# Kernel optimization log

Measured on AMD Instinct MI355X. Metric: run time of the kernel, lower is better.

The kernel has to match this reference:

```python
import jax, jax.numpy as jnp
import numpy as np
from jax import lax

HEADS = 8
WIN_SIZES = (2, 4, 8)


def _linear(x, w, b):
    return x @ w + b


def _window_attention(x2d, ws, w4, b4):
    # x2d: (B,H,W,C); w4: (4,C,C) = [q,k,v,out]; b4: (4,C)
    B, H, W, C = x2d.shape
    p1, p2 = H // ws, W // ws
    xw = x2d.reshape(B, p1, ws, p2, ws, C).transpose(0, 1, 3, 2, 4, 5)
    xw = xw.reshape(B, p1, p2, ws * ws, C)
    hs = C // HEADS
    q = _linear(xw, w4[0], b4[0]).reshape(B, p1, p2, ws * ws, HEADS, hs)
    k = _linear(xw, w4[1], b4[1]).reshape(B, p1, p2, ws * ws, HEADS, hs)
    v = _linear(xw, w4[2], b4[2]).reshape(B, p1, p2, ws * ws, HEADS, hs)
    scores = jnp.einsum('bpqwhd,bpqvhd->bpqhwv', q, k) / jnp.sqrt(jnp.asarray(hs, x2d.dtype))
    probs = jax.nn.softmax(scores, axis=-1)
    ctx = jnp.einsum('bpqhwv,bpqvhd->bpqwhd', probs, v).reshape(B, p1, p2, ws * ws, C)
    return _linear(ctx, w4[3], b4[3])


def _unwindow(out, ws):
    B, p1, p2, win, C = out.shape
    s = out.reshape(B, p1, p2, ws, ws, C).transpose(0, 1, 3, 2, 4, 5)
    return s.reshape(B, p1 * ws, p2 * ws, C)


def _up_bilinear_ac(x, oh, ow):
    # x: (B,C,h,w); bilinear with align_corners=True (UpsamplingBilinear2d)
    B, C, h, w = x.shape
    def grid(o, i):
        pos = jnp.arange(o, dtype=x.dtype) * ((i - 1) / (o - 1))
        i0 = jnp.floor(pos).astype(jnp.int32)
        i1 = jnp.minimum(i0 + 1, i - 1)
        return i0, i1, pos - i0.astype(x.dtype)
    r0, r1, tr = grid(oh, h)
    c0, c1, tc = grid(ow, w)
    xr = x[:, :, r0, :] * (1 - tr)[None, None, :, None] + x[:, :, r1, :] * tr[None, None, :, None]
    return xr[:, :, :, c0] * (1 - tc) + xr[:, :, :, c1] * tc


def _forward(x, attn_w, attn_b, edge_w, mlp_w1, mlp_b1, mlp_w2, mlp_b2,
             dl_w, dl_b, ax_w, ax_b, g_shift, g_bias, sq_w, sq_b):
    B, N, C = x.shape
    H = W = int(np.sqrt(N))
    x2d = x.reshape(B, H, W, C)

    # multi-scale window attention branches
    scale_outputs = [_unwindow(_window_attention(x2d, ws, attn_w[i], attn_b[i]), ws)
                     for i, ws in enumerate(WIN_SIZES)]

    # adaptive window selector
    xc = x2d.transpose(0, 3, 1, 2)  # (B,C,H,W)
    edge = jnp.abs(lax.conv_general_dilated(xc, edge_w, (1, 1), 'SAME'))
    avg = lax.reduce_window(edge, 0.0, lax.add, (1, 1, 3, 3), (1, 1, 1, 1), 'SAME') / 9.0
    e = avg.transpose(0, 2, 3, 1)  # (B,H,W,1)
    wts = jax.nn.softmax(jax.nn.relu(e @ mlp_w1 + mlp_b1) @ mlp_w2 + mlp_b2, axis=-1)

    blended = sum(wts[..., i:i + 1] * scale_outputs[i] for i in range(len(WIN_SIZES)))
    h_map = blended.transpose(0, 3, 1, 2)  # (B,C,H,W)

    # ws=4 window attention -> DlightConv token pooling
    x_win = _window_attention(x2d, 4, attn_w[1], attn_b[1])  # (B,p,p,16,C)
    probs = jax.nn.softmax(jnp.mean(x_win, axis=-2) @ dl_w + dl_b, axis=-1)
    x_dl = jnp.sum(x_win * probs[..., None], axis=-2)  # (B,p,p,C)

    # axial attention (no head split, no scaling in the axial branch)
    q = _linear(x_dl, ax_w[0], ax_b[0])
    k = _linear(x_dl, ax_w[1], ax_b[1])
    v = _linear(x_dl, ax_w[2], ax_b[2])
    scores_x = jnp.einsum('bhwc,bhvc->bhwv', q, k)  # (B,r,c,k)
    scores_y = jnp.einsum('bhwc,bvwc->bwhv', q, k)  # (B,c,r,k)

    # GaussianTrans: vectorized per-pixel gaussian positional bias
    p = x_dl.shape[1]
    idx = jnp.arange(p, dtype=x.dtype)
    dist2 = (idx[None, :] - idx[:, None]) ** 2          # [pos, k]
    gb = -(g_shift[0] * dist2 + g_bias[0])              # (p,p)
    ax = jax.nn.softmax(scores_x + gb[None, None, :, :], axis=-1)       # bias indexed by c
    ay = jax.nn.softmax(jnp.swapaxes(scores_y, 1, 2) + gb[None, :, None, :], axis=-1)  # bias by r
    x_g = jnp.einsum('brck,brkd->brcd', ax, v) + jnp.einsum('brck,bkcd->brcd', ay, v)

    x_g = _up_bilinear_ac(x_g.transpose(0, 3, 1, 2), H, W)  # (B,C,H,W)

    cat = jnp.concatenate([x_g, h_map], axis=1)  # (B,2C,H,W)
    out = jnp.einsum('oc,bchw->bohw', sq_w, cat) + sq_b[None, :, None, None]
    return out.transpose(0, 2, 3, 1).reshape(B, N, C)


def setup_inputs() -> dict:
    key = jax.random.key(0)
    ks = jax.random.split(key, 16)
    B, N, C = 16, 4096, 256
    s = 0.02
    return {
        'x': jax.random.normal(ks[0], (B, N, C), jnp.float32),
        'attn_w': jax.random.normal(ks[1], (3, 4, C, C), jnp.float32) * s,
        'attn_b': jax.random.normal(ks[2], (3, 4, C), jnp.float32) * s,
        'edge_w': jax.random.normal(ks[3], (1, C, 3, 3), jnp.float32) * s,
        'mlp_w1': jax.random.normal(ks[4], (1, 16), jnp.float32) * s,
        'mlp_b1': jax.random.normal(ks[5], (16,), jnp.float32) * s,
        'mlp_w2': jax.random.normal(ks[6], (16, 3), jnp.float32) * s,
        'mlp_b2': jax.random.normal(ks[7], (3,), jnp.float32) * s,
        'dl_w': jax.random.normal(ks[8], (C, 16), jnp.float32) * s,
        'dl_b': jax.random.normal(ks[9], (16,), jnp.float32) * s,
        'ax_w': jax.random.normal(ks[10], (3, C, C), jnp.float32) * s,
        'ax_b': jax.random.normal(ks[11], (3, C), jnp.float32) * s,
        'g_shift': jnp.abs(jax.random.normal(ks[12], (1,), jnp.float32)),
        'g_bias': -jnp.abs(jax.random.normal(ks[13], (1,), jnp.float32)),
        'sq_w': jax.random.normal(ks[14], (C, 2 * C), jnp.float32) * s,
        'sq_b': jax.random.normal(ks[15], (C,), jnp.float32) * s,
    }


def reference(x, attn_w, attn_b, edge_w, mlp_w1, mlp_b1, mlp_w2, mlp_b2,
              dl_w, dl_b, ax_w, ax_b, g_shift, g_bias, sq_w, sq_b):
    return _forward(x, attn_w, attn_b, edge_w, mlp_w1, mlp_b1, mlp_w2, mlp_b2,
                    dl_w, dl_b, ax_w, ax_b, g_shift, g_bias, sq_w, sq_b)
```

## Files before the change

### kernel.cpp

```cpp
#include <hip/hip_runtime.h>
#include <math.h>


#define CHUNK_B 4
#define CHUNK_TOK (CHUNK_B * 4096)
#define KS 32

typedef __attribute__((ext_vector_type(8))) short short8;
typedef __attribute__((ext_vector_type(8))) unsigned short ushort8;
typedef __attribute__((ext_vector_type(4))) float f32x4;

__device__ __forceinline__ ushort f2bf(float f) {
    union { float f; unsigned u; } v; v.f = f;
    unsigned r = v.u + 0x7fff + ((v.u >> 16) & 1);
    return (ushort)(r >> 16);
}
__device__ __forceinline__ float bf2f(ushort h) {
    union { unsigned u; float f; } v; v.u = ((unsigned)h) << 16; return v.f;
}
__device__ __forceinline__ void split2(float v, ushort& h, ushort& l) {
    h = f2bf(v);
    l = f2bf(v - bf2f(h));
}

__device__ __forceinline__ void gld16(const ushort* g, ushort* l) {
    __builtin_amdgcn_global_load_lds(
        (const __attribute__((address_space(1))) unsigned int*)g,
        (__attribute__((address_space(3))) unsigned int*)l,
        16, 0, 0);
}

__global__ __launch_bounds__(256) void split_w_kmajor(
    const float* __restrict__ W, ushort* __restrict__ Th, ushort* __restrict__ Tl, int nmats)
{
    const int idx = blockIdx.x * 256 + threadIdx.x;
    if (idx >= nmats * 65536) return;
    const int mat = idx >> 16, r = idx & 65535;
    const int n = r >> 8, k = r & 255;
    const float v = W[(size_t)mat * 65536 + k * 256 + n];
    ushort h, l; split2(v, h, l);
    Th[idx] = h; Tl[idx] = l;
}
__global__ __launch_bounds__(256) void split_w_nmajor(
    const float* __restrict__ W, ushort* __restrict__ Th, ushort* __restrict__ Tl, int total)
{
    const int idx = blockIdx.x * 256 + threadIdx.x;
    if (idx >= total) return;
    ushort h, l; split2(W[idx], h, l);
    Th[idx] = h; Tl[idx] = l;
}

#define GEMM_DECLS                                                            \
    __shared__ ushort Ah[128 * KS], Al[128 * KS], Bh[128 * KS], Bl[128 * KS]; \
    const int tid = threadIdx.x;                                              \
    const int wave = tid >> 6, lane = tid & 63;                               \
    const int quad = lane >> 4, l16 = lane & 15;                              \
    const int wr = (wave >> 1) * 64, wc = (wave & 1) * 64;                    \
    f32x4 acc[4][4];                                                          \
    _Pragma("unroll") for (int i = 0; i < 4; i++)                             \
        _Pragma("unroll") for (int j = 0; j < 4; j++)                         \
            acc[i][j] = (f32x4){0.f, 0.f, 0.f, 0.f};

#define STAGE_GLD(dstbuf, srcp, strideE, rowbase, k0e)                        \
    _Pragma("unroll") for (int jj = 0; jj < 2; jj++) {                        \
        const int rr = (wave << 5) + (jj << 4) + (lane >> 2);                 \
        const int kqs = (lane & 3) ^ ((lane >> 3) & 3);                       \
        gld16((srcp) + (size_t)((rowbase) + rr) * (strideE) + (k0e) + (kqs << 3), \
              (dstbuf) + (wave << 10) + (jj << 9));                           \
    }

#define STAGE_F32(AhD, AlD, Aptr, kk)                                         \
    _Pragma("unroll") for (int cc = 0; cc < 2; cc++) {                        \
        const int ch = tid + cc * 256;                                        \
        const int r = ch >> 2, kq = ch & 3;                                   \
        const int wsl = (kq ^ ((r >> 1) & 3)) * 8;                            \
        const float* p = (Aptr) + (size_t)(m0 + r) * 256 + (kk) + kq * 8;     \
        const float4 v0 = *(const float4*)p;                                  \
        const float4 v1 = *(const float4*)(p + 4);                            \
        ushort8 h, l; ushort hh, ll;                                          \
        split2(v0.x, hh, ll); h[0] = hh; l[0] = ll;                           \
        split2(v0.y, hh, ll); h[1] = hh; l[1] = ll;                           \
        split2(v0.z, hh, ll); h[2] = hh; l[2] = ll;                           \
        split2(v0.w, hh, ll); h[3] = hh; l[3] = ll;                           \
        split2(v1.x, hh, ll); h[4] = hh; l[4] = ll;                           \
        split2(v1.y, hh, ll); h[5] = hh; l[5] = ll;                           \
        split2(v1.z, hh, ll); h[6] = hh; l[6] = ll;                           \
        split2(v1.w, hh, ll); h[7] = hh; l[7] = ll;                           \
        *(ushort8*)&(AhD)[r * KS + wsl] = h;                                  \
        *(ushort8*)&(AlD)[r * KS + wsl] = l;                                  \
    }

#define GEMM_COMPUTE                                                          \
    {                                                                         \
        const int aswz = (l16 & 6) << 2;                  \
        short8 afh[4], afl[4], bfh[4], bfl[4];                                \
        _Pragma("unroll") for (int i = 0; i < 4; i++) {                       \
            const int ro = (wr + i * 16 + l16) * KS + ((quad * 8) ^ aswz);    \
            afh[i] = *(const short8*)&Ah[ro];                                 \
            afl[i] = *(const short8*)&Al[ro];                                 \
        }                                                                     \
        _Pragma("unroll") for (int j = 0; j < 4; j++) {                       \
            const int no = (wc + j * 16 + l16) * KS + ((quad * 8) ^ aswz);    \
            bfh[j] = *(const short8*)&Bh[no];                                 \
            bfl[j] = *(const short8*)&Bl[no];                                 \
        }                                                                     \
        _Pragma("unroll") for (int i = 0; i < 4; i++)                         \
            _Pragma("unroll") for (int j = 0; j < 4; j++) {                   \
                acc[i][j] = __builtin_amdgcn_mfma_f32_16x16x32_bf16(          \
                    afh[i], bfh[j], acc[i][j], 0, 0, 0);                      \
                acc[i][j] = __builtin_amdgcn_mfma_f32_16x16x32_bf16(          \
                    afl[i], bfh[j], acc[i][j], 0, 0, 0);                      \
                acc[i][j] = __builtin_amdgcn_mfma_f32_16x16x32_bf16(          \
                    afh[i], bfl[j], acc[i][j], 0, 0, 0);                      \
            }                                                                 \
    }

__global__ __launch_bounds__(256, 2) void gemm3_mfma(
    const ushort* __restrict__ AgH, const ushort* __restrict__ AgL,
    const ushort* __restrict__ Wth, const ushort* __restrict__ Wtl,
    const float* __restrict__ b0, const float* __restrict__ b1, const float* __restrict__ b2,
    float* __restrict__ O0, float* __restrict__ O1, float* __restrict__ O2)
{
    const int m0 = blockIdx.x * 128;
    const int mat = blockIdx.y >> 1;
    const int col0 = (blockIdx.y & 1) * 128;
    const ushort* wth = Wth + (size_t)mat * 65536 + (size_t)col0 * 256;
    const ushort* wtl = Wtl + (size_t)mat * 65536 + (size_t)col0 * 256;
    GEMM_DECLS
    for (int k0 = 0; k0 < 256; k0 += 32) {
        STAGE_GLD(Ah, AgH, 256, m0, k0)
        STAGE_GLD(Al, AgL, 256, m0, k0)
        STAGE_GLD(Bh, wth, 256, 0, k0)
        STAGE_GLD(Bl, wtl, 256, 0, k0)
        __syncthreads();
        GEMM_COMPUTE
        __syncthreads();
    }
    const float* bias = (mat == 0) ? b0 : (mat == 1) ? b1 : b2;
    float* O = (mat == 0) ? O0 : (mat == 1) ? O1 : O2;
#pragma unroll
    for (int j = 0; j < 4; j++) {
        const int col = col0 + wc + j * 16 + l16;
        const float bj = bias[col];
#pragma unroll
        for (int i = 0; i < 4; i++) {
            const int rbase = m0 + wr + i * 16 + quad * 4;
#pragma unroll
            for (int r = 0; r < 4; r++)
                O[(size_t)(rbase + r) * 256 + col] = acc[i][j][r] + bj;
        }
    }
}

__global__ __launch_bounds__(256, 2) void gemmp_mfma(
    const ushort* __restrict__ AgH, const ushort* __restrict__ AgL,
    const ushort* __restrict__ Wth, const ushort* __restrict__ Wtl,
    const float* __restrict__ bias,
    float* __restrict__ Sout, int store_s,
    float* __restrict__ Blnd, const float* __restrict__ wts, int scale_idx, int blend_init,
    int row_off)
{
    const int m0 = blockIdx.x * 128;
    const int col0 = blockIdx.y * 128;
    const ushort* wth = Wth + (size_t)col0 * 256;
    const ushort* wtl = Wtl + (size_t)col0 * 256;
    GEMM_DECLS
    for (int k0 = 0; k0 < 256; k0 += 32) {
        STAGE_GLD(Ah, AgH, 256, m0, k0)
        STAGE_GLD(Al, AgL, 256, m0, k0)
        STAGE_GLD(Bh, wth, 256, 0, k0)
        STAGE_GLD(Bl, wtl, 256, 0, k0)
        __syncthreads();
        GEMM_COMPUTE
        __syncthreads();
    }
#pragma unroll
    for (int i = 0; i < 4; i++) {
        const int rbase = m0 + wr + i * 16 + quad * 4;
#pragma unroll
        for (int r = 0; r < 4; r++) {
            const size_t grow = (size_t)row_off + rbase + r;
            const float wt = wts[grow * 3 + scale_idx];
#pragma unroll
            for (int j = 0; j < 4; j++) {
                const int col = col0 + wc + j * 16 + l16;
                const float v = acc[i][j][r] + bias[col];
                if (store_s) Sout[grow * 256 + col] = v;
                float* bp = Blnd + grow * 256 + col;
                if (blend_init) *bp = wt * v;
                else            *bp = *bp + wt * v;
            }
        }
    }
}

__global__ __launch_bounds__(256, 2) void gemmf_mfma(
    const ushort* __restrict__ UPH, const ushort* __restrict__ UPL,
    const float* __restrict__ BLD,
    const ushort* __restrict__ Wth, const ushort* __restrict__ Wtl,
    const float* __restrict__ SQB, float* __restrict__ OUT)
{
    const int m0 = blockIdx.x * 128;
    const int col0 = blockIdx.y * 128;
    const ushort* wth = Wth + (size_t)col0 * 512;
    const ushort* wtl = Wtl + (size_t)col0 * 512;
    GEMM_DECLS
    for (int k0 = 0; k0 < 512; k0 += 32) {
        if (k0 < 256) {
            STAGE_GLD(Ah, UPH, 256, m0, k0)
            STAGE_GLD(Al, UPL, 256, m0, k0)
        } else {
            STAGE_F32(Ah, Al, BLD, (k0 & 255))
        }
        STAGE_GLD(Bh, wth, 512, 0, k0)
        STAGE_GLD(Bl, wtl, 512, 0, k0)
        __syncthreads();
        GEMM_COMPUTE
        __syncthreads();
    }
#pragma unroll
    for (int j = 0; j < 4; j++) {
        const int col = col0 + wc + j * 16 + l16;
        const float bj = SQB[col];
#pragma unroll
        for (int i = 0; i < 4; i++) {
            const int rbase = m0 + wr + i * 16 + quad * 4;
#pragma unroll
            for (int r = 0; r < 4; r++)
                OUT[(size_t)(rbase + r) * 256 + col] = acc[i][j][r] + bj;
        }
    }
}

template <int WS, int NH>
__global__ __launch_bounds__(256) void win_attn(
    const float* __restrict__ Q, const float* __restrict__ K,
    const float* __restrict__ V, ushort* __restrict__ CTXh, ushort* __restrict__ CTXl)
{
    constexpr int WIN = WS * WS;
    constexpr int NW = 64 / WS;
    constexpr int CW = NH * 32;
    __shared__ float qs[WIN][CW + 4], ks[WIN][CW + 4], vs[WIN][CW + 4];
    __shared__ float sc[NH][WIN][WIN + 1];
    const int tid = threadIdx.x;
    const int wid = blockIdx.x;
    const int b = wid / (NW * NW);
    const int rem = wid % (NW * NW);
    const int p = rem / NW, q = rem % NW;
    const int h0 = blockIdx.y * NH;

    for (int idx = tid; idx < WIN * CW; idx += 256) {
        const int i = idx / CW;
        const int cc = idx % CW;
        const int ti = i / WS, tj = i % WS;
        const size_t g = ((size_t)(b * 4096 + (p * WS + ti) * 64 + (q * WS + tj))) * 256 + h0 * 32 + cc;
        qs[i][cc] = Q[g]; ks[i][cc] = K[g]; vs[i][cc] = V[g];
    }
    __syncthreads();
    const float scale = 0.17677669529663687f;
    for (int idx = tid; idx < NH * WIN * WIN; idx += 256) {
        const int hl = idx / (WIN * WIN);
        const int r = idx % (WIN * WIN);
        const int i = r / WIN, j = r % WIN;
        const int co = hl * 32;
        float s = 0.f;
#pragma unroll
        for (int d = 0; d < 32; d++) s += qs[i][co + d] * ks[j][co + d];
        sc[hl][i][j] = s * scale;
    }
    __syncthreads();
    if (tid < NH * WIN) {
        const int hl = tid / WIN, i = tid % WIN;
        float mx = -3.4e38f;
        for (int j = 0; j < WIN; j++) mx = fmaxf(mx, sc[hl][i][j]);
        float sum = 0.f;
        for (int j = 0; j < WIN; j++) {
            float e = __expf(sc[hl][i][j] - mx);
            sc[hl][i][j] = e; sum += e;
        }
        const float inv = 1.f / sum;
        for (int j = 0; j < WIN; j++) sc[hl][i][j] *= inv;
    }
    __syncthreads();
    for (int idx = tid; idx < WIN * CW; idx += 256) {
        const int i = idx / CW;
        const int cc = idx % CW;
        const int hl = cc >> 5;
        float s = 0.f;
        for (int j = 0; j < WIN; j++) s += sc[hl][i][j] * vs[j][cc];
        const int ti = i / WS, tj = i % WS;
        const size_t g = ((size_t)(b * 4096 + (p * WS + ti) * 64 + (q * WS + tj))) * 256 + h0 * 32 + cc;
        ushort hh, ll; split2(s, hh, ll);
        CTXh[g] = hh; CTXl[g] = ll;
    }
}

__global__ __launch_bounds__(256) void edge_gemm9(
    const float* __restrict__ x, const float* __restrict__ ew, float* __restrict__ ytmp,
    ushort* __restrict__ Xh, ushort* __restrict__ Xl)
{
    __shared__ float wsm[2304];
    const int tid = threadIdx.x;
    for (int i = tid; i < 2304; i += 256) wsm[i] = ew[i];
    __syncthreads();
    const int wave = tid >> 6, lane = tid & 63;
    const int p = blockIdx.x * 4 + wave;
    const float4 xv = *(const float4*)(x + (size_t)p * 256 + lane * 4);
    {
        ushort4 h4, l4;
        split2(xv.x, h4.x, l4.x); split2(xv.y, h4.y, l4.y);
        split2(xv.z, h4.z, l4.z); split2(xv.w, h4.w, l4.w);
        *(ushort4*)(Xh + (size_t)p * 256 + lane * 4) = h4;
        *(ushort4*)(Xl + (size_t)p * 256 + lane * 4) = l4;
    }
    float acc[9];
#pragma unroll
    for (int t = 0; t < 9; t++) acc[t] = 0.f;
    const float xs[4] = {xv.x, xv.y, xv.z, xv.w};
#pragma unroll
    for (int i = 0; i < 4; i++) {
        const int c = lane * 4 + i;
#pragma unroll
        for (int t = 0; t < 9; t++)
            acc[t] = fmaf(xs[i], wsm[c * 9 + t], acc[t]);
    }
#pragma unroll
    for (int t = 0; t < 9; t++) {
#pragma unroll
        for (int off = 1; off < 64; off <<= 1)
            acc[t] += __shfl_xor(acc[t], off);
    }
    if (lane < 9) {
        float v = acc[0];
        switch (lane) {
            case 1: v = acc[1]; break; case 2: v = acc[2]; break;
            case 3: v = acc[3]; break; case 4: v = acc[4]; break;
            case 5: v = acc[5]; break; case 6: v = acc[6]; break;
            case 7: v = acc[7]; break; case 8: v = acc[8]; break;
            default: break;
        }
        ytmp[(size_t)p * 9 + lane] = v;
    }
}

__global__ __launch_bounds__(256) void edge_combine(
    const float* __restrict__ ytmp, float* __restrict__ edge)
{
    const int idx = blockIdx.x * 256 + threadIdx.x;
    const int b = idx >> 12, rem = idx & 4095, h = rem >> 6, w = rem & 63;
    float s = 0.f;
#pragma unroll
    for (int kh = 0; kh < 3; kh++) {
        const int hh = h + kh - 1;
        if ((unsigned)hh > 63u) continue;
#pragma unroll
        for (int kw = 0; kw < 3; kw++) {
            const int ww = w + kw - 1;
            if ((unsigned)ww > 63u) continue;
            s += ytmp[((size_t)b * 4096 + hh * 64 + ww) * 9 + kh * 3 + kw];
        }
    }
    edge[idx] = fabsf(s);
}

__global__ __launch_bounds__(256) void avg_mlp(
    const float* __restrict__ edge, const float* __restrict__ w1, const float* __restrict__ b1,
    const float* __restrict__ w2, const float* __restrict__ b2, float* __restrict__ wts)
{
    const int idx = blockIdx.x * 256 + threadIdx.x;
    const int b = idx >> 12, rem = idx & 4095, h = rem >> 6, w = rem & 63;
    float s = 0.f;
#pragma unroll
    for (int kh = -1; kh <= 1; kh++) {
        const int hh = h + kh;
        if ((unsigned)hh > 63u) continue;
#pragma unroll
        for (int kw = -1; kw <= 1; kw++) {
            const int ww = w + kw;
            if ((unsigned)ww > 63u) continue;
            s += edge[(size_t)b * 4096 + hh * 64 + ww];
        }
    }
    const float e = s / 9.f;
    float l0 = b2[0], l1 = b2[1], l2 = b2[2];
#pragma unroll
    for (int j = 0; j < 16; j++) {
        float hd = fmaxf(e * w1[j] + b1[j], 0.f);
        l0 += hd * w2[j * 3 + 0];
        l1 += hd * w2[j * 3 + 1];
        l2 += hd * w2[j * 3 + 2];
    }
    const float mx = fmaxf(l0, fmaxf(l1, l2));
    const float e0 = __expf(l0 - mx), e1 = __expf(l1 - mx), e2 = __expf(l2 - mx);
    const float inv = 1.f / (e0 + e1 + e2);
    wts[(size_t)idx * 3 + 0] = e0 * inv;
    wts[(size_t)idx * 3 + 1] = e1 * inv;
    wts[(size_t)idx * 3 + 2] = e2 * inv;
}

__global__ __launch_bounds__(256) void dlight(
    const float* __restrict__ S1, const float* __restrict__ dlw,
    const float* __restrict__ dlb, ushort* __restrict__ XDLH, ushort* __restrict__ XDLL)
{
    __shared__ float xw[16][257];
    __shared__ float m[256];
    __shared__ float pr[16];
    __shared__ float pr2[16];
    const int wid = blockIdx.x;
    const int b = wid >> 8, rem = wid & 255, p = rem >> 4, q = rem & 15;
    const int tid = threadIdx.x;
#pragma unroll
    for (int t = 0; t < 16; t++) {
        const int ti = t >> 2, tj = t & 3;
        xw[t][tid] = S1[((size_t)b * 4096 + (p * 4 + ti) * 64 + (q * 4 + tj)) * 256 + tid];
    }
    float mm = 0.f;
#pragma unroll
    for (int t = 0; t < 16; t++) mm += xw[t][tid];
    m[tid] = mm * (1.f / 16.f);
    __syncthreads();
    if (tid < 16) {
        float lg = dlb[tid];
        for (int c = 0; c < 256; c++) lg += m[c] * dlw[c * 16 + tid];
        pr[tid] = lg;
    }
    __syncthreads();
    if (tid < 16) {
        float mx = -3.4e38f;
        for (int j = 0; j < 16; j++) mx = fmaxf(mx, pr[j]);
        float sum = 0.f;
        for (int j = 0; j < 16; j++) sum += __expf(pr[j] - mx);
        pr2[tid] = __expf(pr[tid] - mx) / sum;
    }
    __syncthreads();
    float o = 0.f;
#pragma unroll
    for (int t = 0; t < 16; t++) o += xw[t][tid] * pr2[t];
    ushort hh, ll; split2(o, hh, ll);
    XDLH[(size_t)wid * 256 + tid] = hh;
    XDLL[(size_t)wid * 256 + tid] = ll;
}

__global__ __launch_bounds__(256) void axial_row(
    const float* __restrict__ Q, const float* __restrict__ K, const float* __restrict__ V,
    const float* __restrict__ gsp, const float* __restrict__ gbp, float* __restrict__ XG)
{
    __shared__ float qs[16][257], ks[16][257], vs[16][257];
    __shared__ float sc[16][17];
    const int bid = blockIdx.x;
    const int b = bid >> 4, r = bid & 15;
    const int tid = threadIdx.x;
    const float gs = gsp[0], gb = gbp[0];
#pragma unroll
    for (int w = 0; w < 16; w++) {
        const size_t base = ((size_t)b * 256 + r * 16 + w) * 256 + tid;
        qs[w][tid] = Q[base]; ks[w][tid] = K[base]; vs[w][tid] = V[base];
    }
    __syncthreads();
    {
        const int w = tid >> 4, vv = tid & 15;
        float s = 0.f;
        for (int c = 0; c < 256; c++) s += qs[w][c] * ks[vv][c];
        const float d = (float)(w - vv);
        sc[w][vv] = s - (gs * d * d + gb);
    }
    __syncthreads();
    if (tid < 16) {
        float mx = -3.4e38f;
        for (int j = 0; j < 16; j++) mx = fmaxf(mx, sc[tid][j]);
        float sum = 0.f;
        for (int j = 0; j < 16; j++) {
            float e = __expf(sc[tid][j] - mx);
            sc[tid][j] = e; sum += e;
        }
        const float inv = 1.f / sum;
        for (int j = 0; j < 16; j++) sc[tid][j] *= inv;
    }
    __syncthreads();
#pragma unroll
    for (int w2 = 0; w2 < 16; w2++) {
        float o = 0.f;
#pragma unroll
        for (int k2 = 0; k2 < 16; k2++) o += sc[w2][k2] * vs[k2][tid];
        XG[((size_t)b * 256 + r * 16 + w2) * 256 + tid] = o;
    }
}

__global__ __launch_bounds__(256) void axial_col(
    const float* __restrict__ Q, const float* __restrict__ K, const float* __restrict__ V,
    const float* __restrict__ gsp, const float* __restrict__ gbp, float* __restrict__ XG)
{
    __shared__ float qs[16][257], ks[16][257], vs[16][257];
    __shared__ float sc[16][17];
    const int bid = blockIdx.x;
    const int b = bid >> 4, col = bid & 15;
    const int tid = threadIdx.x;
    const float gs = gsp[0], gb = gbp[0];
#pragma unroll
    for (int h = 0; h < 16; h++) {
        const size_t base = ((size_t)b * 256 + h * 16 + col) * 256 + tid;
        qs[h][tid] = Q[base]; ks[h][tid] = K[base]; vs[h][tid] = V[base];
    }
    __syncthreads();
    {
        const int r = tid >> 4, vv = tid & 15;
        float s = 0.f;
        for (int c = 0; c < 256; c++) s += qs[r][c] * ks[vv][c];
        const float d = (float)(r - vv);
        sc[r][vv] = s - (gs * d * d + gb);
    }
    __syncthreads();
    if (tid < 16) {
        float mx = -3.4e38f;
        for (int j = 0; j < 16; j++) mx = fmaxf(mx, sc[tid][j]);
        float sum = 0.f;
        for (int j = 0; j < 16; j++) {
            float e = __expf(sc[tid][j] - mx);
            sc[tid][j] = e; sum += e;
        }
        const float inv = 1.f / sum;
        for (int j = 0; j < 16; j++) sc[tid][j] *= inv;
    }
    __syncthreads();
#pragma unroll
    for (int r2 = 0; r2 < 16; r2++) {
        float o = 0.f;
#pragma unroll
        for (int k2 = 0; k2 < 16; k2++) o += sc[r2][k2] * vs[k2][tid];
        XG[((size_t)b * 256 + r2 * 16 + col) * 256 + tid] += o;
    }
}

__global__ __launch_bounds__(256) void upsample(
    const float* __restrict__ XG, ushort* __restrict__ UPH, ushort* __restrict__ UPL)
{
    const unsigned idx = blockIdx.x * 256u + threadIdx.x;
    const int c = idx & 255;
    const unsigned t2 = idx >> 8;
    const int w = t2 & 63;
    const unsigned t3 = t2 >> 6;
    const int h = t3 & 63;
    const int b = t3 >> 6;
    const float rr = 15.f / 63.f;
    const float ph = h * rr, pw = w * rr;
    int h0 = (int)floorf(ph); float th = ph - (float)h0; int h1 = min(h0 + 1, 15);
    int w0 = (int)floorf(pw); float tw = pw - (float)w0; int w1 = min(w0 + 1, 15);
    const size_t bb = (size_t)b * 256;
    const float v00 = XG[((bb + h0 * 16 + w0)) * 256 + c];
    const float v10 = XG[((bb + h1 * 16 + w0)) * 256 + c];
    const float v01 = XG[((bb + h0 * 16 + w1)) * 256 + c];
    const float v11 = XG[((bb + h1 * 16 + w1)) * 256 + c];
    const float c0 = v00 * (1.f - th) + v10 * th;
    const float c1 = v01 * (1.f - th) + v11 * th;
    const float val = c0 * (1.f - tw) + c1 * tw;
    ushort hh, ll; split2(val, hh, ll);
    UPH[idx] = hh; UPL[idx] = ll;
}

extern "C" void kernel_launch(void* const* d_in, const int* in_sizes, int n_in,
                              void* d_out, int out_size, void* d_ws, size_t ws_size,
                              hipStream_t stream)
{
    const float* x      = (const float*)d_in[0];
    const float* attn_w = (const float*)d_in[1];
    const float* attn_b = (const float*)d_in[2];
    const float* edge_w = (const float*)d_in[3];
    const float* mlp_w1 = (const float*)d_in[4];
    const float* mlp_b1 = (const float*)d_in[5];
    const float* mlp_w2 = (const float*)d_in[6];
    const float* mlp_b2 = (const float*)d_in[7];
    const float* dl_w   = (const float*)d_in[8];
    const float* dl_b   = (const float*)d_in[9];
    const float* ax_w   = (const float*)d_in[10];
    const float* ax_b   = (const float*)d_in[11];
    const float* g_shift= (const float*)d_in[12];
    const float* g_bias = (const float*)d_in[13];
    const float* sq_w   = (const float*)d_in[14];
    const float* sq_b   = (const float*)d_in[15];
    float* out = (float*)d_out;

    float* ws = (float*)d_ws;
    const size_t MT = 65536;
    float* blend = ws;
    float* s1    = blend + MT * 256;
    float* scr   = s1 + MT * 256;
    float* chQ   = scr;
    float* chK   = chQ + (size_t)CHUNK_TOK * 256;
    float* chV   = chK + (size_t)CHUNK_TOK * 256;
    ushort* ctxh = (ushort*)(chV + (size_t)CHUNK_TOK * 256);
    ushort* ctxl = ctxh + (size_t)CHUNK_TOK * 256;
    ushort* uph  = (ushort*)scr;
    ushort* upl  = uph + MT * 256;
    float* ytmp  = scr;
    float* edge  = scr + MT * 256;
    float* wts   = edge + 65536;
    float* xdl   = wts + 196608;
    ushort* xdlh = (ushort*)xdl;
    ushort* xdll = xdlh + 1048576;
    float* axq   = xdl + 1048576;
    float* axk   = axq + 1048576;
    float* axv   = axk + 1048576;
    float* xg    = axv + 1048576;
    ushort* Wth = (ushort*)(xg + 1048576);
    ushort* Wtl = Wth + 1114112;
    ushort* xh = (ushort*)out;
    ushort* xl = xh + MT * 256;

    split_w_kmajor<<<(12 * 65536 + 255) / 256, 256, 0, stream>>>(attn_w, Wth, Wtl, 12);
    split_w_kmajor<<<(3 * 65536 + 255) / 256, 256, 0, stream>>>(
        ax_w, Wth + (size_t)12 * 65536, Wtl + (size_t)12 * 65536, 3);
    split_w_nmajor<<<(131072 + 255) / 256, 256, 0, stream>>>(
        sq_w, Wth + (size_t)15 * 65536, Wtl + (size_t)15 * 65536, 131072);

    edge_gemm9<<<16384, 256, 0, stream>>>(x, edge_w, ytmp, xh, xl);
    edge_combine<<<256, 256, 0, stream>>>(ytmp, edge);
    avg_mlp<<<256, 256, 0, stream>>>(edge, mlp_w1, mlp_b1, mlp_w2, mlp_b2, wts);

    for (int i = 0; i < 3; i++) {
        const ushort* Wh = Wth + (size_t)i * 4 * 65536;
        const ushort* Wl = Wtl + (size_t)i * 4 * 65536;
        const float* c0 = attn_b + (size_t)(i * 4 + 0) * 256;
        const float* c1 = attn_b + (size_t)(i * 4 + 1) * 256;
        const float* c2 = attn_b + (size_t)(i * 4 + 2) * 256;
        const float* c3 = attn_b + (size_t)(i * 4 + 3) * 256;
        for (int ch = 0; ch < 16 / CHUNK_B; ch++) {
            const size_t toff = (size_t)ch * CHUNK_TOK;
            gemm3_mfma<<<dim3(CHUNK_TOK / 128, 6), 256, 0, stream>>>(
                xh + toff * 256, xl + toff * 256, Wh, Wl, c0, c1, c2, chQ, chK, chV);
            if (i == 0)
                win_attn<2, 8><<<dim3(CHUNK_B * 32 * 32, 1), 256, 0, stream>>>(chQ, chK, chV, ctxh, ctxl);
            if (i == 1)
                win_attn<4, 4><<<dim3(CHUNK_B * 16 * 16, 2), 256, 0, stream>>>(chQ, chK, chV, ctxh, ctxl);
            if (i == 2)
                win_attn<8, 1><<<dim3(CHUNK_B * 8 * 8, 8), 256, 0, stream>>>(chQ, chK, chV, ctxh, ctxl);
            gemmp_mfma<<<dim3(CHUNK_TOK / 128, 2), 256, 0, stream>>>(
                ctxh, ctxl, Wh + (size_t)3 * 65536, Wl + (size_t)3 * 65536, c3,
                s1, (i == 1) ? 1 : 0, blend, wts, i, (i == 0) ? 1 : 0, (int)toff);
        }
    }

    dlight<<<4096, 256, 0, stream>>>(s1, dl_w, dl_b, xdlh, xdll);

    gemm3_mfma<<<dim3(4096 / 128, 6), 256, 0, stream>>>(
        xdlh, xdll, Wth + (size_t)12 * 65536, Wtl + (size_t)12 * 65536,
        ax_b, ax_b + 256, ax_b + 512, axq, axk, axv);
    axial_row<<<256, 256, 0, stream>>>(axq, axk, axv, g_shift, g_bias, xg);
    axial_col<<<256, 256, 0, stream>>>(axq, axk, axv, g_shift, g_bias, xg);

    upsample<<<65536, 256, 0, stream>>>(xg, uph, upl);

    gemmf_mfma<<<dim3(512, 2), 256, 0, stream>>>(
        uph, upl, blend, Wth + (size_t)15 * 65536, Wtl + (size_t)15 * 65536, sq_b, out);
}
```

Before: 1.300 ms.

## Merge weight split and edge kernels, swizzle GEMM blocks, use register LDS staging

Merges the three weight-split kernels into one launch and fuses edge_combine with avg_mlp into a single edge_sel kernel that keeps edge tiles in shared memory. The GEMMs drop global_load_lds in favour of plain 16-byte vector loads followed by LDS stores. The 2D grid becomes a 1D grid with an XCD-style block remap so neighbouring blocks share A/B tiles in cache. The chunk and scale loops are swapped so each token chunk stays hot across the three scales. These cut launch overhead and DRAM traffic, but the register-staged loads may cost more instructions than direct-to-LDS loads.

Measured after the change: 1.291 ms. About the same (-0.8%).

```diff
diff --git a/kernel.cpp b/kernel.cpp
--- a/kernel.cpp
+++ b/kernel.cpp
@@ -23,30 +23,26 @@
     l = f2bf(v - bf2f(h));
 }
 
-__device__ __forceinline__ void gld16(const ushort* g, ushort* l) {
-    __builtin_amdgcn_global_load_lds(
-        (const __attribute__((address_space(1))) unsigned int*)g,
-        (__attribute__((address_space(3))) unsigned int*)l,
-        16, 0, 0);
-}
-
-__global__ __launch_bounds__(256) void split_w_kmajor(
-    const float* __restrict__ W, ushort* __restrict__ Th, ushort* __restrict__ Tl, int nmats)
+__global__ __launch_bounds__(256) void split_w_all(
+    const float* __restrict__ AW, const float* __restrict__ XW,
+    const float* __restrict__ SW, ushort* __restrict__ Th, ushort* __restrict__ Tl)
 {
     const int idx = blockIdx.x * 256 + threadIdx.x;
-    if (idx >= nmats * 65536) return;
-    const int mat = idx >> 16, r = idx & 65535;
-    const int n = r >> 8, k = r & 255;
-    const float v = W[(size_t)mat * 65536 + k * 256 + n];
+    if (idx >= 1114112) return;
+    float v;
+    if (idx < 786432) {
+        const int mat = idx >> 16, r = idx & 65535;
+        const int n = r >> 8, k = r & 255;
+        v = AW[(size_t)mat * 65536 + k * 256 + n];
+    } else if (idx < 983040) {
+        const int j = idx - 786432;
+        const int mat = j >> 16, r = j & 65535;
+        const int n = r >> 8, k = r & 255;
+        v = XW[(size_t)mat * 65536 + k * 256 + n];
+    } else {
+        v = SW[idx - 983040];
+    }
     ushort h, l; split2(v, h, l);
-    Th[idx] = h; Tl[idx] = l;
-}
-__global__ __launch_bounds__(256) void split_w_nmajor(
-    const float* __restrict__ W, ushort* __restrict__ Th, ushort* __restrict__ Tl, int total)
-{
-    const int idx = blockIdx.x * 256 + threadIdx.x;
-    if (idx >= total) return;
-    ushort h, l; split2(W[idx], h, l);
     Th[idx] = h; Tl[idx] = l;
 }
 
@@ -61,12 +57,13 @@
         _Pragma("unroll") for (int j = 0; j < 4; j++)                         \
             acc[i][j] = (f32x4){0.f, 0.f, 0.f, 0.f};
 
-#define STAGE_GLD(dstbuf, srcp, strideE, rowbase, k0e)                        \
-    _Pragma("unroll") for (int jj = 0; jj < 2; jj++) {                        \
-        const int rr = (wave << 5) + (jj << 4) + (lane >> 2);                 \
-        const int kqs = (lane & 3) ^ ((lane >> 3) & 3);                       \
-        gld16((srcp) + (size_t)((rowbase) + rr) * (strideE) + (k0e) + (kqs << 3), \
-              (dstbuf) + (wave << 10) + (jj << 9));                           \
+#define STAGE_US(dst, src, strideE, rowbase, k0e)                             \
+    _Pragma("unroll") for (int cc = 0; cc < 2; cc++) {                        \
+        const int ch_ = tid + cc * 256;                                       \
+        const int r_ = ch_ >> 2;                                              \
+        const int kq_ = (ch_ & 3) ^ ((r_ >> 1) & 3);                          \
+        *(ushort8*)&(dst)[ch_ * 8] = *(const ushort8*)((src) +                \
+            (size_t)((rowbase) + r_) * (strideE) + (k0e) + (kq_ << 3));       \
     }
 
 #define STAGE_F32(AhD, AlD, Aptr, kk)                                         \
@@ -121,17 +118,21 @@
     const float* __restrict__ b0, const float* __restrict__ b1, const float* __restrict__ b2,
     float* __restrict__ O0, float* __restrict__ O1, float* __restrict__ O2)
 {
-    const int m0 = blockIdx.x * 128;
-    const int mat = blockIdx.y >> 1;
-    const int col0 = (blockIdx.y & 1) * 128;
+    const int nq = gridDim.x >> 3;
+    const int bid = blockIdx.x;
+    const int lid = (bid & 7) * nq + (bid >> 3);
+    const int m0 = (lid / 6) * 128;
+    const int ymat = lid % 6;
+    const int mat = ymat >> 1;
+    const int col0 = (ymat & 1) * 128;
     const ushort* wth = Wth + (size_t)mat * 65536 + (size_t)col0 * 256;
     const ushort* wtl = Wtl + (size_t)mat * 65536 + (size_t)col0 * 256;
     GEMM_DECLS
     for (int k0 = 0; k0 < 256; k0 += 32) {
-        STAGE_GLD(Ah, AgH, 256, m0, k0)
-        STAGE_GLD(Al, AgL, 256, m0, k0)
-        STAGE_GLD(Bh, wth, 256, 0, k0)
-        STAGE_GLD(Bl, wtl, 256, 0, k0)
+        STAGE_US(Ah, AgH, 256, m0, k0)
+        STAGE_US(Al, AgL, 256, m0, k0)
+        STAGE_US(Bh, wth, 256, 0, k0)
+        STAGE_US(Bl, wtl, 256, 0, k0)
         __syncthreads();
         GEMM_COMPUTE
         __syncthreads();
@@ -160,16 +161,19 @@
     float* __restrict__ Blnd, const float* __restrict__ wts, int scale_idx, int blend_init,
     int row_off)
 {
-    const int m0 = blockIdx.x * 128;
-    const int col0 = blockIdx.y * 128;
+    const int nq = gridDim.x >> 3;
+    const int bid = blockIdx.x;
+    const int lid = (bid & 7) * nq + (bid >> 3);
+    const int m0 = (lid >> 1) * 128;
+    const int col0 = (lid & 1) * 128;
     const ushort* wth = Wth + (size_t)col0 * 256;
     const ushort* wtl = Wtl + (size_t)col0 * 256;
     GEMM_DECLS
     for (int k0 = 0; k0 < 256; k0 += 32) {
-        STAGE_GLD(Ah, AgH, 256, m0, k0)
-        STAGE_GLD(Al, AgL, 256, m0, k0)
-        STAGE_GLD(Bh, wth, 256, 0, k0)
-        STAGE_GLD(Bl, wtl, 256, 0, k0)
+        STAGE_US(Ah, AgH, 256, m0, k0)
+        STAGE_US(Al, AgL, 256, m0, k0)
+        STAGE_US(Bh, wth, 256, 0, k0)
+        STAGE_US(Bl, wtl, 256, 0, k0)
         __syncthreads();
         GEMM_COMPUTE
         __syncthreads();
@@ -200,20 +204,23 @@
     const ushort* __restrict__ Wth, const ushort* __restrict__ Wtl,
     const float* __restrict__ SQB, float* __restrict__ OUT)
 {
-    const int m0 = blockIdx.x * 128;
-    const int col0 = blockIdx.y * 128;
+    const int nq = gridDim.x >> 3;
+    const int bid = blockIdx.x;
+    const int lid = (bid & 7) * nq + (bid >> 3);
+    const int m0 = (lid >> 1) * 128;
+    const int col0 = (lid & 1) * 128;
     const ushort* wth = Wth + (size_t)col0 * 512;
     const ushort* wtl = Wtl + (size_t)col0 * 512;
     GEMM_DECLS
     for (int k0 = 0; k0 < 512; k0 += 32) {
         if (k0 < 256) {
-            STAGE_GLD(Ah, UPH, 256, m0, k0)
-            STAGE_GLD(Al, UPL, 256, m0, k0)
+            STAGE_US(Ah, UPH, 256, m0, k0)
+            STAGE_US(Al, UPL, 256, m0, k0)
         } else {
             STAGE_F32(Ah, Al, BLD, (k0 & 255))
         }
-        STAGE_GLD(Bh, wth, 512, 0, k0)
-        STAGE_GLD(Bl, wtl, 512, 0, k0)
+        STAGE_US(Bh, wth, 512, 0, k0)
+        STAGE_US(Bl, wtl, 512, 0, k0)
         __syncthreads();
         GEMM_COMPUTE
         __syncthreads();
@@ -343,42 +350,49 @@
     }
 }
 
-__global__ __launch_bounds__(256) void edge_combine(
-    const float* __restrict__ ytmp, float* __restrict__ edge)
-{
-    const int idx = blockIdx.x * 256 + threadIdx.x;
-    const int b = idx >> 12, rem = idx & 4095, h = rem >> 6, w = rem & 63;
+__global__ __launch_bounds__(256) void edge_sel(
+    const float* __restrict__ ytmp,
+    const float* __restrict__ w1, const float* __restrict__ b1,
+    const float* __restrict__ w2, const float* __restrict__ b2,
+    float* __restrict__ wts)
+{
+    __shared__ float esm[6][65];
+    const int tid = threadIdx.x;
+    const int bid = blockIdx.x;
+    const int b = bid >> 4;
+    const int rblk = (bid & 15) * 4;
+    for (int idx = tid; idx < 6 * 64; idx += 256) {
+        const int er = idx >> 6, ew = idx & 63;
+        const int hh = rblk + er - 1;
+        float e = 0.f;
+        if ((unsigned)hh <= 63u) {
+            float s = 0.f;
+#pragma unroll
+            for (int kh = 0; kh < 3; kh++) {
+                const int hy = hh + kh - 1;
+                if ((unsigned)hy > 63u) continue;
+#pragma unroll
+                for (int kw = 0; kw < 3; kw++) {
+                    const int wy = ew + kw - 1;
+                    if ((unsigned)wy > 63u) continue;
+                    s += ytmp[((size_t)b * 4096 + hy * 64 + wy) * 9 + kh * 3 + kw];
+                }
+            }
+            e = fabsf(s);
+        }
+        esm[er][ew] = e;
+    }
+    __syncthreads();
+    const int lh = tid >> 6, w = tid & 63;
+    const int h = rblk + lh;
     float s = 0.f;
 #pragma unroll
     for (int kh = 0; kh < 3; kh++) {
-        const int hh = h + kh - 1;
-        if ((unsigned)hh > 63u) continue;
 #pragma unroll
         for (int kw = 0; kw < 3; kw++) {
             const int ww = w + kw - 1;
             if ((unsigned)ww > 63u) continue;
-            s += ytmp[((size_t)b * 4096 + hh * 64 + ww) * 9 + kh * 3 + kw];
-        }
-    }
-    edge[idx] = fabsf(s);
-}
-
-__global__ __launch_bounds__(256) void avg_mlp(
-    const float* __restrict__ edge, const float* __restrict__ w1, const float* __restrict__ b1,
-    const float* __restrict__ w2, const float* __restrict__ b2, float* __restrict__ wts)
-{
-    const int idx = blockIdx.x * 256 + threadIdx.x;
-    const int b = idx >> 12, rem = idx & 4095, h = rem >> 6, w = rem & 63;
-    float s = 0.f;
-#pragma unroll
-    for (int kh = -1; kh <= 1; kh++) {
-        const int hh = h + kh;
-        if ((unsigned)hh > 63u) continue;
-#pragma unroll
-        for (int kw = -1; kw <= 1; kw++) {
-            const int ww = w + kw;
-            if ((unsigned)ww > 63u) continue;
-            s += edge[(size_t)b * 4096 + hh * 64 + ww];
+            s += esm[lh + kh][ww];
         }
     }
     const float e = s / 9.f;
@@ -393,9 +407,10 @@
     const float mx = fmaxf(l0, fmaxf(l1, l2));
     const float e0 = __expf(l0 - mx), e1 = __expf(l1 - mx), e2 = __expf(l2 - mx);
     const float inv = 1.f / (e0 + e1 + e2);
-    wts[(size_t)idx * 3 + 0] = e0 * inv;
-    wts[(size_t)idx * 3 + 1] = e1 * inv;
-    wts[(size_t)idx * 3 + 2] = e2 * inv;
+    const size_t gidx = (size_t)b * 4096 + h * 64 + w;
+    wts[gidx * 3 + 0] = e0 * inv;
+    wts[gidx * 3 + 1] = e1 * inv;
+    wts[gidx * 3 + 2] = e2 * inv;
 }
 
 __global__ __launch_bounds__(256) void dlight(
@@ -592,8 +607,7 @@
     ushort* uph  = (ushort*)scr;
     ushort* upl  = uph + MT * 256;
     float* ytmp  = scr;
-    float* edge  = scr + MT * 256;
-    float* wts   = edge + 65536;
+    float* wts   = scr + MT * 256 + 65536;
     float* xdl   = wts + 196608;
     ushort* xdlh = (ushort*)xdl;
     ushort* xdll = xdlh + 1048576;
@@ -606,26 +620,22 @@
     ushort* xh = (ushort*)out;
     ushort* xl = xh + MT * 256;
 
-    split_w_kmajor<<<(12 * 65536 + 255) / 256, 256, 0, stream>>>(attn_w, Wth, Wtl, 12);
-    split_w_kmajor<<<(3 * 65536 + 255) / 256, 256, 0, stream>>>(
-        ax_w, Wth + (size_t)12 * 65536, Wtl + (size_t)12 * 65536, 3);
-    split_w_nmajor<<<(131072 + 255) / 256, 256, 0, stream>>>(
-        sq_w, Wth + (size_t)15 * 65536, Wtl + (size_t)15 * 65536, 131072);
+    split_w_all<<<(1114112 + 255) / 256, 256, 0, stream>>>(
+        attn_w, ax_w, sq_w, Wth, Wtl);
 
     edge_gemm9<<<16384, 256, 0, stream>>>(x, edge_w, ytmp, xh, xl);
-    edge_combine<<<256, 256, 0, stream>>>(ytmp, edge);
-    avg_mlp<<<256, 256, 0, stream>>>(edge, mlp_w1, mlp_b1, mlp_w2, mlp_b2, wts);
-
-    for (int i = 0; i < 3; i++) {
-        const ushort* Wh = Wth + (size_t)i * 4 * 65536;
-        const ushort* Wl = Wtl + (size_t)i * 4 * 65536;
-        const float* c0 = attn_b + (size_t)(i * 4 + 0) * 256;
-        const float* c1 = attn_b + (size_t)(i * 4 + 1) * 256;
-        const float* c2 = attn_b + (size_t)(i * 4 + 2) * 256;
-        const float* c3 = attn_b + (size_t)(i * 4 + 3) * 256;
-        for (int ch = 0; ch < 16 / CHUNK_B; ch++) {
-            const size_t toff = (size_t)ch * CHUNK_TOK;
-            gemm3_mfma<<<dim3(CHUNK_TOK / 128, 6), 256, 0, stream>>>(
+    edge_sel<<<256, 256, 0, stream>>>(ytmp, mlp_w1, mlp_b1, mlp_w2, mlp_b2, wts);
+
+    for (int ch = 0; ch < 16 / CHUNK_B; ch++) {
+        const size_t toff = (size_t)ch * CHUNK_TOK;
+        for (int i = 0; i < 3; i++) {
+            const ushort* Wh = Wth + (size_t)i * 4 * 65536;
+            const ushort* Wl = Wtl + (size_t)i * 4 * 65536;
+            const float* c0 = attn_b + (size_t)(i * 4 + 0) * 256;
+            const float* c1 = attn_b + (size_t)(i * 4 + 1) * 256;
+            const float* c2 = attn_b + (size_t)(i * 4 + 2) * 256;
+            const float* c3 = attn_b + (size_t)(i * 4 + 3) * 256;
+            gemm3_mfma<<<CHUNK_TOK / 128 * 6, 256, 0, stream>>>(
                 xh + toff * 256, xl + toff * 256, Wh, Wl, c0, c1, c2, chQ, chK, chV);
             if (i == 0)
                 win_attn<2, 8><<<dim3(CHUNK_B * 32 * 32, 1), 256, 0, stream>>>(chQ, chK, chV, ctxh, ctxl);
@@ -633,7 +643,7 @@
                 win_attn<4, 4><<<dim3(CHUNK_B * 16 * 16, 2), 256, 0, stream>>>(chQ, chK, chV, ctxh, ctxl);
             if (i == 2)
                 win_attn<8, 1><<<dim3(CHUNK_B * 8 * 8, 8), 256, 0, stream>>>(chQ, chK, chV, ctxh, ctxl);
-            gemmp_mfma<<<dim3(CHUNK_TOK / 128, 2), 256, 0, stream>>>(
+            gemmp_mfma<<<CHUNK_TOK / 128 * 2, 256, 0, stream>>>(
                 ctxh, ctxl, Wh + (size_t)3 * 65536, Wl + (size_t)3 * 65536, c3,
                 s1, (i == 1) ? 1 : 0, blend, wts, i, (i == 0) ? 1 : 0, (int)toff);
         }
@@ -641,7 +651,7 @@
 
     dlight<<<4096, 256, 0, stream>>>(s1, dl_w, dl_b, xdlh, xdll);
 
-    gemm3_mfma<<<dim3(4096 / 128, 6), 256, 0, stream>>>(
+    gemm3_mfma<<<4096 / 128 * 6, 256, 0, stream>>>(
         xdlh, xdll, Wth + (size_t)12 * 65536, Wtl + (size_t)12 * 65536,
         ax_b, ax_b + 256, ax_b + 512, axq, axk, axv);
     axial_row<<<256, 256, 0, stream>>>(axq, axk, axv, g_shift, g_bias, xg);
@@ -649,6 +659,6 @@
 
     upsample<<<65536, 256, 0, stream>>>(xg, uph, upl);
 
-    gemmf_mfma<<<dim3(512, 2), 256, 0, stream>>>(
+    gemmf_mfma<<<1024, 256, 0, stream>>>(
         uph, upl, blend, Wth + (size_t)15 * 65536, Wtl + (size_t)15 * 65536, sq_b, out);
 }
```
